# Kernel optimization log

Hardware: AMD Instinct MI355X
Metric: run time of the kernel (lower is better)

## Reference

```python
import jax, jax.numpy as jnp
import numpy as np

NUM_INSTANCES = 64  # instance ids 1..64; 0 is background


def setup_inputs() -> dict:
    key = jax.random.key(0)
    k1, k2 = jax.random.split(key)
    H = W = 1024
    pred_mask = jax.random.randint(k1, (H, W), 0, NUM_INSTANCES + 1, dtype=jnp.int32)
    true_mask = jax.random.randint(k2, (H, W), 0, NUM_INSTANCES + 1, dtype=jnp.int32)
    return {"pred_mask": pred_mask, "true_mask": true_mask}


def reference(pred_mask, true_mask):
    # One-hot per-instance binary masks, flattened over pixels: [K, H*W]
    ids = jnp.arange(1, NUM_INSTANCES + 1, dtype=pred_mask.dtype)
    P = (pred_mask.reshape(-1)[None, :] == ids[:, None]).astype(jnp.float32)
    T = (true_mask.reshape(-1)[None, :] == ids[:, None]).astype(jnp.float32)

    # Pairwise intersection via matmul (replaces nested numpy loops): [K, K]
    inter = jnp.einsum('pn,tn->pt', P, T)
    area_p = P.sum(axis=1)  # [K]
    area_t = T.sum(axis=1)  # [K]
    union = area_p[:, None] + area_t[None, :] - inter
    # original: iou = 0 when union == 0
    iou = jnp.where(union > 0, inter / jnp.maximum(union, 1.0), 0.0)

    # Instances with zero area correspond to ids absent from the mask; the
    # original skips them entirely. An absent instance contributes iou=0 to
    # every pair, so it never affects the max; we only exclude it from the
    # loss sum / instance count.
    present_p = area_p > 0
    present_t = area_t > 0

    max_iou_p = jnp.max(iou, axis=1)  # best true match per pred instance
    max_iou_t = jnp.max(iou, axis=0)  # best pred match per true instance

    loss_sum = (jnp.sum(jnp.where(present_p, 1.0 - max_iou_p, 0.0))
                + jnp.sum(jnp.where(present_t, 1.0 - max_iou_t, 0.0)))
    num_instances = (jnp.sum(present_p.astype(jnp.float32))
                     + jnp.sum(present_t.astype(jnp.float32)))
    return jnp.where(num_instances > 0, loss_sum / jnp.maximum(num_instances, 1.0), 0.0)
```

## Files before the change

kernel.cpp:

```cpp
#include <hip/hip_runtime.h>

#define NUM_IDS 64
#define NB 65
#define HIST_BINS (NB * NB)

__global__ __launch_bounds__(256) void isl_hist_kernel(
    const int* __restrict__ pred, const int* __restrict__ tru,
    int* __restrict__ ghist, int n4) {
    __shared__ int lhist[HIST_BINS];
    for (int i = threadIdx.x; i < HIST_BINS; i += blockDim.x) lhist[i] = 0;
    __syncthreads();

    const int4* __restrict__ p4 = (const int4*)pred;
    const int4* __restrict__ t4 = (const int4*)tru;
    int idx = blockIdx.x * blockDim.x + threadIdx.x;
    int stride = gridDim.x * blockDim.x;
    for (int i = idx; i < n4; i += stride) {
        int4 p = p4[i];
        int4 t = t4[i];
        atomicAdd(&lhist[p.x * NB + t.x], 1);
        atomicAdd(&lhist[p.y * NB + t.y], 1);
        atomicAdd(&lhist[p.z * NB + t.z], 1);
        atomicAdd(&lhist[p.w * NB + t.w], 1);
    }
    __syncthreads();

    for (int i = threadIdx.x; i < HIST_BINS; i += blockDim.x) {
        int v = lhist[i];
        if (v) atomicAdd(&ghist[i], v);
    }
}

__global__ __launch_bounds__(256) void isl_reduce_kernel(
    const int* __restrict__ ghist, float* __restrict__ out) {
    __shared__ int C[HIST_BINS];
    __shared__ float ap[NUM_IDS], at[NUM_IDS];
    __shared__ float rowmax[NUM_IDS], colmax[NUM_IDS];

    for (int i = threadIdx.x; i < HIST_BINS; i += blockDim.x) C[i] = ghist[i];
    __syncthreads();

    int t = threadIdx.x;
    if (t < NUM_IDS) {
        int s = 0;
        for (int j = 0; j < NB; ++j) s += C[(t + 1) * NB + j];
        ap[t] = (float)s;
        int s2 = 0;
        for (int i = 0; i < NB; ++i) s2 += C[i * NB + (t + 1)];
        at[t] = (float)s2;
    }
    __syncthreads();

    if (t < NUM_IDS) {
        float a = ap[t];
        float m = 0.f;
        for (int j = 0; j < NUM_IDS; ++j) {
            float inter = (float)C[(t + 1) * NB + (j + 1)];
            float uni = a + at[j] - inter;
            float iou = (uni > 0.f) ? inter / uni : 0.f;
            m = fmaxf(m, iou);
        }
        rowmax[t] = m;

        float b = at[t];
        float m2 = 0.f;
        for (int i = 0; i < NUM_IDS; ++i) {
            float inter = (float)C[(i + 1) * NB + (t + 1)];
            float uni = ap[i] + b - inter;
            float iou = (uni > 0.f) ? inter / uni : 0.f;
            m2 = fmaxf(m2, iou);
        }
        colmax[t] = m2;
    }
    __syncthreads();

    if (t == 0) {
        float loss = 0.f, cnt = 0.f;
        for (int i = 0; i < NUM_IDS; ++i) {
            if (ap[i] > 0.f) { loss += 1.f - rowmax[i]; cnt += 1.f; }
            if (at[i] > 0.f) { loss += 1.f - colmax[i]; cnt += 1.f; }
        }
        out[0] = (cnt > 0.f) ? loss / cnt : 0.f;
    }
}

extern "C" void kernel_launch(void* const* d_in, const int* in_sizes, int n_in,
                              void* d_out, int out_size, void* d_ws, size_t ws_size,
                              hipStream_t stream) {
    const int* pred = (const int*)d_in[0];
    const int* tru  = (const int*)d_in[1];
    float* out = (float*)d_out;
    int n = in_sizes[0];
    int* ghist = (int*)d_ws;

    hipMemsetAsync(ghist, 0, HIST_BINS * sizeof(int), stream);
    isl_hist_kernel<<<128, 256, 0, stream>>>(pred, tru, ghist, n >> 2);
    isl_reduce_kernel<<<1, 256, 0, stream>>>(ghist, out);
}
```

Measured before the change: 42.77 us.

## Replace global atomic histogram merge with per-block partials reduced in final kernel

Each histogram block now writes its full shared-memory joint histogram to a per-block slot in workspace, and the single reduce block sums the 32 partials with int4 loads. This drops the memset and the global atomics. The grid also shrinks from 128×256 to 32×512 threads, and the main loop is restructured with a full-stride unrolled body plus a tail. The trade-off is far fewer blocks to stream 8 MB of input, which may underutilize the GPU's many CUs and memory bandwidth.

```diff
diff --git a/kernel.cpp b/kernel.cpp
--- a/kernel.cpp
+++ b/kernel.cpp
@@ -3,44 +3,65 @@
 #define NUM_IDS 64
 #define NB 65
 #define HIST_BINS (NB * NB)
+#define PADBINS 4228
+#define GROUPS (PADBINS / 4)
+#define HB 32
+#define HT 512
 
-__global__ __launch_bounds__(256) void isl_hist_kernel(
+__global__ __launch_bounds__(HT) void isl_hist_kernel(
     const int* __restrict__ pred, const int* __restrict__ tru,
-    int* __restrict__ ghist, int n4) {
-    __shared__ int lhist[HIST_BINS];
-    for (int i = threadIdx.x; i < HIST_BINS; i += blockDim.x) lhist[i] = 0;
+    int* __restrict__ part, int n4) {
+    __shared__ int lh[PADBINS];
+    for (int i = threadIdx.x; i < PADBINS; i += HT) lh[i] = 0;
     __syncthreads();
 
     const int4* __restrict__ p4 = (const int4*)pred;
     const int4* __restrict__ t4 = (const int4*)tru;
-    int idx = blockIdx.x * blockDim.x + threadIdx.x;
-    int stride = gridDim.x * blockDim.x;
-    for (int i = idx; i < n4; i += stride) {
+    int idx = blockIdx.x * HT + threadIdx.x;
+    const int stride = HB * HT;
+    int nfull = n4 / stride;
+    int i = idx;
+#pragma unroll 4
+    for (int k = 0; k < nfull; ++k, i += stride) {
         int4 p = p4[i];
         int4 t = t4[i];
-        atomicAdd(&lhist[p.x * NB + t.x], 1);
-        atomicAdd(&lhist[p.y * NB + t.y], 1);
-        atomicAdd(&lhist[p.z * NB + t.z], 1);
-        atomicAdd(&lhist[p.w * NB + t.w], 1);
+        atomicAdd(&lh[p.x * NB + t.x], 1);
+        atomicAdd(&lh[p.y * NB + t.y], 1);
+        atomicAdd(&lh[p.z * NB + t.z], 1);
+        atomicAdd(&lh[p.w * NB + t.w], 1);
+    }
+    if (i < n4) {
+        int4 p = p4[i];
+        int4 t = t4[i];
+        atomicAdd(&lh[p.x * NB + t.x], 1);
+        atomicAdd(&lh[p.y * NB + t.y], 1);
+        atomicAdd(&lh[p.z * NB + t.z], 1);
+        atomicAdd(&lh[p.w * NB + t.w], 1);
     }
     __syncthreads();
 
-    for (int i = threadIdx.x; i < HIST_BINS; i += blockDim.x) {
-        int v = lhist[i];
-        if (v) atomicAdd(&ghist[i], v);
-    }
+    int base = blockIdx.x * PADBINS;
+    for (int j = threadIdx.x; j < PADBINS; j += HT) part[base + j] = lh[j];
 }
 
-__global__ __launch_bounds__(256) void isl_reduce_kernel(
-    const int* __restrict__ ghist, float* __restrict__ out) {
-    __shared__ int C[HIST_BINS];
+__global__ __launch_bounds__(1024) void isl_reduce_kernel(
+    const int* __restrict__ part, float* __restrict__ out) {
+    __shared__ alignas(16) int C[PADBINS];
     __shared__ float ap[NUM_IDS], at[NUM_IDS];
     __shared__ float rowmax[NUM_IDS], colmax[NUM_IDS];
 
-    for (int i = threadIdx.x; i < HIST_BINS; i += blockDim.x) C[i] = ghist[i];
+    int t = threadIdx.x;
+    for (int g = t; g < GROUPS; g += 1024) {
+        int4 s = make_int4(0, 0, 0, 0);
+#pragma unroll 8
+        for (int b = 0; b < HB; ++b) {
+            const int4 v = *(const int4*)(part + b * PADBINS + (g << 2));
+            s.x += v.x; s.y += v.y; s.z += v.z; s.w += v.w;
+        }
+        *(int4*)(&C[g << 2]) = s;
+    }
     __syncthreads();
 
-    int t = threadIdx.x;
     if (t < NUM_IDS) {
         int s = 0;
         for (int j = 0; j < NB; ++j) s += C[(t + 1) * NB + j];
@@ -91,9 +112,8 @@
     const int* tru  = (const int*)d_in[1];
     float* out = (float*)d_out;
     int n = in_sizes[0];
-    int* ghist = (int*)d_ws;
+    int* part = (int*)d_ws;
 
-    hipMemsetAsync(ghist, 0, HIST_BINS * sizeof(int), stream);
-    isl_hist_kernel<<<128, 256, 0, stream>>>(pred, tru, ghist, n >> 2);
-    isl_reduce_kernel<<<1, 256, 0, stream>>>(ghist, out);
+    isl_hist_kernel<<<HB, HT, 0, stream>>>(pred, tru, part, n >> 2);
+    isl_reduce_kernel<<<1, 1024, 0, stream>>>(part, out);
 }
```

Result: faster. 38.44 us, median of 2 (-10.1%).

## Fuse histogram and IoU reduction into one kernel with last-block finalize

Applied to the files above, without the earlier changes.

Merges the histogram and reduction kernels into a single launch in which the last block to finish, detected through an atomic counter and thread fences, computes the IoU loss. It also doubles the grid to 256 blocks and unrolls the main loop four times so more loads are in flight. This removes one kernel launch and its gap but adds a counter atomic, fences, and more global atomic merges from the extra blocks.

```diff
diff --git a/kernel.cpp b/kernel.cpp
--- a/kernel.cpp
+++ b/kernel.cpp
@@ -3,82 +3,118 @@
 #define NUM_IDS 64
 #define NB 65
 #define HIST_BINS (NB * NB)
+#define G 256
+#define T 256
 
-__global__ __launch_bounds__(256) void isl_hist_kernel(
+__global__ __launch_bounds__(T) void isl_fused_kernel(
     const int* __restrict__ pred, const int* __restrict__ tru,
-    int* __restrict__ ghist, int n4) {
-    __shared__ int lhist[HIST_BINS];
-    for (int i = threadIdx.x; i < HIST_BINS; i += blockDim.x) lhist[i] = 0;
+    int* __restrict__ ghist, int* __restrict__ counter,
+    float* __restrict__ out, int n4) {
+    __shared__ int lh[HIST_BINS];
+    __shared__ float ap[NUM_IDS], at[NUM_IDS];
+    __shared__ float rowmax[NUM_IDS], colmax[NUM_IDS];
+    __shared__ int is_last;
+
+    const int tid = threadIdx.x;
+    for (int i = tid; i < HIST_BINS; i += T) lh[i] = 0;
     __syncthreads();
 
     const int4* __restrict__ p4 = (const int4*)pred;
     const int4* __restrict__ t4 = (const int4*)tru;
-    int idx = blockIdx.x * blockDim.x + threadIdx.x;
-    int stride = gridDim.x * blockDim.x;
-    for (int i = idx; i < n4; i += stride) {
+    const int stride = G * T;
+    int idx = blockIdx.x * T + tid;
+
+    int nfull = n4 / stride;
+    int i = idx;
+    while (nfull >= 4) {
+        int4 pa = p4[i];            int4 ta = t4[i];
+        int4 pb = p4[i + stride];   int4 tb = t4[i + stride];
+        int4 pc = p4[i + 2*stride]; int4 tc = t4[i + 2*stride];
+        int4 pd = p4[i + 3*stride]; int4 td = t4[i + 3*stride];
+        atomicAdd(&lh[pa.x * NB + ta.x], 1);
+        atomicAdd(&lh[pa.y * NB + ta.y], 1);
+        atomicAdd(&lh[pa.z * NB + ta.z], 1);
+        atomicAdd(&lh[pa.w * NB + ta.w], 1);
+        atomicAdd(&lh[pb.x * NB + tb.x], 1);
+        atomicAdd(&lh[pb.y * NB + tb.y], 1);
+        atomicAdd(&lh[pb.z * NB + tb.z], 1);
+        atomicAdd(&lh[pb.w * NB + tb.w], 1);
+        atomicAdd(&lh[pc.x * NB + tc.x], 1);
+        atomicAdd(&lh[pc.y * NB + tc.y], 1);
+        atomicAdd(&lh[pc.z * NB + tc.z], 1);
+        atomicAdd(&lh[pc.w * NB + tc.w], 1);
+        atomicAdd(&lh[pd.x * NB + td.x], 1);
+        atomicAdd(&lh[pd.y * NB + td.y], 1);
+        atomicAdd(&lh[pd.z * NB + td.z], 1);
+        atomicAdd(&lh[pd.w * NB + td.w], 1);
+        i += 4 * stride;
+        nfull -= 4;
+    }
+    for (; i < n4; i += stride) {
         int4 p = p4[i];
         int4 t = t4[i];
-        atomicAdd(&lhist[p.x * NB + t.x], 1);
-        atomicAdd(&lhist[p.y * NB + t.y], 1);
-        atomicAdd(&lhist[p.z * NB + t.z], 1);
-        atomicAdd(&lhist[p.w * NB + t.w], 1);
+        atomicAdd(&lh[p.x * NB + t.x], 1);
+        atomicAdd(&lh[p.y * NB + t.y], 1);
+        atomicAdd(&lh[p.z * NB + t.z], 1);
+        atomicAdd(&lh[p.w * NB + t.w], 1);
     }
     __syncthreads();
 
-    for (int i = threadIdx.x; i < HIST_BINS; i += blockDim.x) {
-        int v = lhist[i];
-        if (v) atomicAdd(&ghist[i], v);
+    for (int b = tid; b < HIST_BINS; b += T) {
+        int v = lh[b];
+        if (v) atomicAdd(&ghist[b], v);
     }
-}
 
-__global__ __launch_bounds__(256) void isl_reduce_kernel(
-    const int* __restrict__ ghist, float* __restrict__ out) {
-    __shared__ int C[HIST_BINS];
-    __shared__ float ap[NUM_IDS], at[NUM_IDS];
-    __shared__ float rowmax[NUM_IDS], colmax[NUM_IDS];
+    __threadfence();
+    if (tid == 0) {
+        int old = atomicAdd(counter, 1);
+        is_last = (old == G - 1);
+    }
+    __syncthreads();
+    if (!is_last) return;
 
-    for (int i = threadIdx.x; i < HIST_BINS; i += blockDim.x) C[i] = ghist[i];
+    __threadfence();
+    for (int b = tid; b < HIST_BINS; b += T) lh[b] = atomicAdd(&ghist[b], 0);
     __syncthreads();
 
-    int t = threadIdx.x;
-    if (t < NUM_IDS) {
+    if (tid < NUM_IDS) {
         int s = 0;
-        for (int j = 0; j < NB; ++j) s += C[(t + 1) * NB + j];
-        ap[t] = (float)s;
+        for (int j = 0; j < NB; ++j) s += lh[(tid + 1) * NB + j];
+        ap[tid] = (float)s;
         int s2 = 0;
-        for (int i = 0; i < NB; ++i) s2 += C[i * NB + (t + 1)];
-        at[t] = (float)s2;
+        for (int k = 0; k < NB; ++k) s2 += lh[k * NB + (tid + 1)];
+        at[tid] = (float)s2;
     }
     __syncthreads();
 
-    if (t < NUM_IDS) {
-        float a = ap[t];
+    if (tid < NUM_IDS) {
+        float a = ap[tid];
         float m = 0.f;
         for (int j = 0; j < NUM_IDS; ++j) {
-            float inter = (float)C[(t + 1) * NB + (j + 1)];
+            float inter = (float)lh[(tid + 1) * NB + (j + 1)];
             float uni = a + at[j] - inter;
             float iou = (uni > 0.f) ? inter / uni : 0.f;
             m = fmaxf(m, iou);
         }
-        rowmax[t] = m;
+        rowmax[tid] = m;
 
-        float b = at[t];
+        float b = at[tid];
         float m2 = 0.f;
-        for (int i = 0; i < NUM_IDS; ++i) {
-            float inter = (float)C[(i + 1) * NB + (t + 1)];
-            float uni = ap[i] + b - inter;
+        for (int k = 0; k < NUM_IDS; ++k) {
+            float inter = (float)lh[(k + 1) * NB + (tid + 1)];
+            float uni = ap[k] + b - inter;
             float iou = (uni > 0.f) ? inter / uni : 0.f;
             m2 = fmaxf(m2, iou);
         }
-        colmax[t] = m2;
+        colmax[tid] = m2;
     }
     __syncthreads();
 
-    if (t == 0) {
+    if (tid == 0) {
         float loss = 0.f, cnt = 0.f;
-        for (int i = 0; i < NUM_IDS; ++i) {
-            if (ap[i] > 0.f) { loss += 1.f - rowmax[i]; cnt += 1.f; }
-            if (at[i] > 0.f) { loss += 1.f - colmax[i]; cnt += 1.f; }
+        for (int k = 0; k < NUM_IDS; ++k) {
+            if (ap[k] > 0.f) { loss += 1.f - rowmax[k]; cnt += 1.f; }
+            if (at[k] > 0.f) { loss += 1.f - colmax[k]; cnt += 1.f; }
         }
         out[0] = (cnt > 0.f) ? loss / cnt : 0.f;
     }
@@ -92,8 +128,8 @@
     float* out = (float*)d_out;
     int n = in_sizes[0];
     int* ghist = (int*)d_ws;
+    int* counter = ghist + HIST_BINS;
 
-    hipMemsetAsync(ghist, 0, HIST_BINS * sizeof(int), stream);
-    isl_hist_kernel<<<128, 256, 0, stream>>>(pred, tru, ghist, n >> 2);
-    isl_reduce_kernel<<<1, 256, 0, stream>>>(ghist, out);
+    hipMemsetAsync(ghist, 0, (HIST_BINS + 1) * sizeof(int), stream);
+    isl_fused_kernel<<<G, T, 0, stream>>>(pred, tru, ghist, counter, out, n >> 2);
 }
```

Measured after the change: 58.34 us. 1.36x slower.
